# Optimization experiments

Measured on AMD Instinct MI355X. Metric: run time of the kernel, lower is better.

The kernel has to match this reference:

```python
import jax, jax.numpy as jnp
import numpy as np

NUM_EMBEDDINGS = 1024
EMBEDDING_SIZE = 256


def setup_inputs() -> dict:
    key = jax.random.key(0)
    k1, k2 = jax.random.split(key)
    z_e = jax.random.normal(k1, (32, 32, 32, EMBEDDING_SIZE), dtype=jnp.float32)
    # original init: uniform(-limit, limit), limit = sqrt(3/num_embeddings)
    limit = np.sqrt(3.0 / NUM_EMBEDDINGS)
    embeddings = jax.random.uniform(
        k2, (NUM_EMBEDDINGS, EMBEDDING_SIZE), dtype=jnp.float32,
        minval=-limit, maxval=limit)
    return {"z_e": z_e, "embeddings": embeddings}


def reference(z_e, embeddings):
    D = embeddings.shape[1]
    z_e_flat = z_e.reshape(-1, D)  # [N, D]
    distances = (
        jnp.sum(z_e_flat * z_e_flat, axis=1, keepdims=True)
        - 2.0 * (z_e_flat @ embeddings.T)
        + jnp.sum(embeddings * embeddings, axis=1)[None, :]
    )  # [N, K]
    z = jnp.argmin(distances, axis=-1).reshape(z_e.shape[:-1])  # indices
    z_q = embeddings[z]  # gather -> same shape as z_e
    return z, z_q
```

## Files before the change

kernel.cpp:

```cpp
#include <hip/hip_runtime.h>
#include <math.h>

#define N_ROWS 32768
#define DIM 256
#define K_CODES 1024
#define MARGIN 2e-3f

typedef float f32x4v __attribute__((ext_vector_type(4)));
typedef short s16x8 __attribute__((ext_vector_type(8)));

#define WS_NEEDED ((size_t)1183748)

__device__ __forceinline__ unsigned short bf16_rne(float f) {
    unsigned int u = __float_as_uint(f);
    unsigned int r = (u + 0x7FFFu + ((u >> 16) & 1u)) >> 16;
    return (unsigned short)r;
}
__device__ __forceinline__ float bf16_f32(unsigned short h) {
    return __uint_as_float(((unsigned int)h) << 16);
}

__device__ __forceinline__ float np_block128_sumsq(const float* e) {
#pragma clang fp contract(off)
    float s[16];
#pragma unroll
    for (int l = 0; l < 16; ++l) {
        float a0 = e[l]       * e[l];
        float a1 = e[16 + l]  * e[16 + l];
        float a2 = e[32 + l]  * e[32 + l];
        float a3 = e[48 + l]  * e[48 + l];
        float a4 = e[64 + l]  * e[64 + l];
        float a5 = e[80 + l]  * e[80 + l];
        float a6 = e[96 + l]  * e[96 + l];
        float a7 = e[112 + l] * e[112 + l];
        s[l] = ((a0 + a1) + (a2 + a3)) + ((a4 + a5) + (a6 + a7));
    }
    float t1[8];
#pragma unroll
    for (int i = 0; i < 8; ++i) t1[i] = s[i] + s[i + 8];
    float t2[4];
#pragma unroll
    for (int i = 0; i < 4; ++i) t2[i] = t1[i] + t1[i + 4];
    return (t2[0] + t2[2]) + (t2[1] + t2[3]);
}

__global__ __launch_bounds__(64) void npsumsq_kernel(const float* __restrict__ src,
                                                     float* __restrict__ dst) {
    __shared__ float buf[16][257];
    const int tid = threadIdx.x;
    const int r0 = blockIdx.x * 16;
#pragma unroll
    for (int it = 0; it < 16; ++it) {
        int idx = it * 64 + tid;
        int r = idx >> 6, c4 = idx & 63;
        float4 v = ((const float4*)(src + (size_t)(r0 + r) * DIM))[c4];
        buf[r][c4 * 4 + 0] = v.x;
        buf[r][c4 * 4 + 1] = v.y;
        buf[r][c4 * 4 + 2] = v.z;
        buf[r][c4 * 4 + 3] = v.w;
    }
    __syncthreads();
    if (tid < 16) {
        const float* e = buf[tid];
        dst[r0 + tid] = np_block128_sumsq(e) + np_block128_sumsq(e + 128);
    }
}

__global__ __launch_bounds__(64) void wprep_kernel(const float* __restrict__ w,
                                                   float* __restrict__ w2,
                                                   unsigned short* __restrict__ wfrag,
                                                   int* __restrict__ flagcnt) {
    __shared__ float buf[16][257];
    const int lane = threadIdx.x;
    const int t = blockIdx.x;
    const int r0 = t * 16;
    if (t == 0 && lane == 0) flagcnt[0] = 0;
#pragma unroll
    for (int it = 0; it < 16; ++it) {
        int idx = it * 64 + lane;
        int r = idx >> 6, c4 = idx & 63;
        float4 v = ((const float4*)(w + (size_t)(r0 + r) * DIM))[c4];
        buf[r][c4 * 4 + 0] = v.x;
        buf[r][c4 * 4 + 1] = v.y;
        buf[r][c4 * 4 + 2] = v.z;
        buf[r][c4 * 4 + 3] = v.w;
    }
    __syncthreads();
    if (lane < 16) {
        const float* e = buf[lane];
        w2[r0 + lane] = np_block128_sumsq(e) + np_block128_sumsq(e + 128);
    }
    const int c = lane & 15, ko = lane >> 4;
#pragma unroll
    for (int q = 0; q < 8; ++q) {
        s16x8 hh, ll;
#pragma unroll
        for (int i = 0; i < 8; ++i) {
            float f = buf[c][q * 32 + ko * 8 + i];
            unsigned short h = bf16_rne(f);
            hh[i] = (short)h;
            ll[i] = (short)bf16_rne(f - bf16_f32(h));
        }
        unsigned short* dh = wfrag + (size_t)t * 8192 + q * 512 + lane * 8;
        *(s16x8*)dh = hh;
        *(s16x8*)(dh + 4096) = ll;
    }
}

__global__ __launch_bounds__(256, 2) void vq_mfma(
    const float* __restrict__ x, const uint4* __restrict__ wfrag4,
    const float* __restrict__ w2g, const float* __restrict__ w,
    float* __restrict__ zout, float* __restrict__ zq,
    int* __restrict__ flagcnt, int* __restrict__ flaglist) {
    __shared__ uint4 tiles[2][1024];
    __shared__ float sw2[K_CODES];
    __shared__ int widx_s[64];

    const int tid = threadIdx.x;
    const int wave = tid >> 6;
    const int lane = tid & 63;
    const int rowblk = blockIdx.x * 64;
    const int rowbase = rowblk + wave * 16;

    for (int i = tid; i < K_CODES; i += 256) sw2[i] = w2g[i];

    s16x8 ahi[8], alo[8];
    {
        const float* xr = x + (size_t)(rowbase + (lane & 15)) * DIM + (lane >> 4) * 8;
#pragma unroll
        for (int q = 0; q < 8; ++q) {
            float4 a = *(const float4*)(xr + q * 32);
            float4 b = *(const float4*)(xr + q * 32 + 4);
            float e[8] = {a.x, a.y, a.z, a.w, b.x, b.y, b.z, b.w};
#pragma unroll
            for (int i = 0; i < 8; ++i) {
                unsigned short h = bf16_rne(e[i]);
                ahi[q][i] = (short)h;
                alo[q][i] = (short)bf16_rne(e[i] - bf16_f32(h));
            }
        }
    }

    tiles[0][tid] = wfrag4[tid];
    tiles[0][tid + 256] = wfrag4[tid + 256];
    tiles[0][tid + 512] = wfrag4[tid + 512];
    tiles[0][tid + 768] = wfrag4[tid + 768];

    float b1[4], b2[4];
    int i1[4];
#pragma unroll
    for (int j = 0; j < 4; ++j) { b1[j] = INFINITY; b2[j] = INFINITY; i1[j] = 0; }

    __syncthreads();

    int cur = 0;
    for (int ct = 0; ct < 64; ++ct) {
        uint4 pf0, pf1, pf2, pf3;
        if (ct < 63) {
            const uint4* g = wfrag4 + (size_t)(ct + 1) * 1024;
            pf0 = g[tid];
            pf1 = g[tid + 256];
            pf2 = g[tid + 512];
            pf3 = g[tid + 768];
        }
        const uint4* th = tiles[cur];
        f32x4v ahh = {0.f, 0.f, 0.f, 0.f};
        f32x4v ahl = {0.f, 0.f, 0.f, 0.f};
        f32x4v alh = {0.f, 0.f, 0.f, 0.f};
#pragma unroll
        for (int q = 0; q < 8; ++q) {
            s16x8 Bh = *(const s16x8*)&th[q * 64 + lane];
            s16x8 Bl = *(const s16x8*)&th[512 + q * 64 + lane];
            ahh = __builtin_amdgcn_mfma_f32_16x16x32_bf16(ahi[q], Bh, ahh, 0, 0, 0);
            ahl = __builtin_amdgcn_mfma_f32_16x16x32_bf16(ahi[q], Bl, ahl, 0, 0, 0);
            alh = __builtin_amdgcn_mfma_f32_16x16x32_bf16(alo[q], Bh, alh, 0, 0, 0);
        }
        const int code = ct * 16 + (lane & 15);
        const float w2v = sw2[code];
#pragma unroll
        for (int j = 0; j < 4; ++j) {
            float d = (ahh[j] + ahl[j]) + alh[j];
            float s = w2v - 2.0f * d;
            if (s < b2[j]) {
                if (s < b1[j]) { b2[j] = b1[j]; b1[j] = s; i1[j] = code; }
                else b2[j] = s;
            }
        }
        if (ct < 63) {
            uint4* d = tiles[cur ^ 1];
            d[tid] = pf0;
            d[tid + 256] = pf1;
            d[tid + 512] = pf2;
            d[tid + 768] = pf3;
            cur ^= 1;
        }
        __syncthreads();
    }

#pragma unroll
    for (int m = 1; m < 16; m <<= 1) {
#pragma unroll
        for (int j = 0; j < 4; ++j) {
            float ov1 = __shfl_xor(b1[j], m);
            int oi = __shfl_xor(i1[j], m);
            float ov2 = __shfl_xor(b2[j], m);
            float nb2 = fminf(fmaxf(b1[j], ov1), fminf(b2[j], ov2));
            if (ov1 < b1[j] || (ov1 == b1[j] && oi < i1[j])) { b1[j] = ov1; i1[j] = oi; }
            b2[j] = nb2;
        }
    }
    if ((lane & 15) == 0) {
#pragma unroll
        for (int j = 0; j < 4; ++j) {
            int rl = wave * 16 + (lane >> 4) * 4 + j;
            widx_s[rl] = i1[j];
            zout[rowblk + rl] = (float)i1[j];
            if (b2[j] - b1[j] < MARGIN) {
                int slot = atomicAdd(flagcnt, 1);
                flaglist[slot] = rowblk + rl;
            }
        }
    }
    __syncthreads();

    const float4* w4 = (const float4*)w;
    float4* zq4 = (float4*)zq;
#pragma unroll
    for (int p = 0; p < 16; ++p) {
        int lin = p * 256 + tid;
        int row = lin >> 6, qq = lin & 63;
        zq4[(size_t)(rowblk + row) * 64 + qq] = w4[(size_t)widx_s[row] * 64 + qq];
    }
}

__global__ __launch_bounds__(256) void rescue_kernel(
    const float* __restrict__ x, const float* __restrict__ w,
    const float* __restrict__ w2g, const int* __restrict__ flagcnt,
    const int* __restrict__ flaglist, float* __restrict__ zout,
    float* __restrict__ zq) {
    __shared__ __align__(16) float xs[DIM];
    __shared__ float dv[256];
    __shared__ int di[256];
    __shared__ int mi_s;
    __shared__ float x2_s;
    const int tid = threadIdx.x;
    const int cnt = flagcnt[0];
    for (int f = blockIdx.x; f < cnt; f += gridDim.x) {
        const int r = flaglist[f];
        __syncthreads();
        for (int i = tid; i < DIM; i += 256) xs[i] = x[(size_t)r * DIM + i];
        __syncthreads();
        if (tid == 0)
            x2_s = np_block128_sumsq(xs) + np_block128_sumsq(xs + 128);
        __syncthreads();
        const float x2vv = x2_s;
        const float4* xs4 = (const float4*)xs;
        const float4* wr0 = (const float4*)(w + (size_t)(tid + 0 * 256) * DIM);
        const float4* wr1 = (const float4*)(w + (size_t)(tid + 1 * 256) * DIM);
        const float4* wr2 = (const float4*)(w + (size_t)(tid + 2 * 256) * DIM);
        const float4* wr3 = (const float4*)(w + (size_t)(tid + 3 * 256) * DIM);
        float acc0 = 0.f, acc1 = 0.f, acc2 = 0.f, acc3 = 0.f;
#pragma unroll 4
        for (int k4 = 0; k4 < DIM / 4; ++k4) {
            float4 xv = xs4[k4];
            float4 w0 = wr0[k4], w1 = wr1[k4], w2 = wr2[k4], w3 = wr3[k4];
            acc0 = __builtin_fmaf(xv.x, w0.x, acc0);
            acc0 = __builtin_fmaf(xv.y, w0.y, acc0);
            acc0 = __builtin_fmaf(xv.z, w0.z, acc0);
            acc0 = __builtin_fmaf(xv.w, w0.w, acc0);
            acc1 = __builtin_fmaf(xv.x, w1.x, acc1);
            acc1 = __builtin_fmaf(xv.y, w1.y, acc1);
            acc1 = __builtin_fmaf(xv.z, w1.z, acc1);
            acc1 = __builtin_fmaf(xv.w, w1.w, acc1);
            acc2 = __builtin_fmaf(xv.x, w2.x, acc2);
            acc2 = __builtin_fmaf(xv.y, w2.y, acc2);
            acc2 = __builtin_fmaf(xv.z, w2.z, acc2);
            acc2 = __builtin_fmaf(xv.w, w2.w, acc2);
            acc3 = __builtin_fmaf(xv.x, w3.x, acc3);
            acc3 = __builtin_fmaf(xv.y, w3.y, acc3);
            acc3 = __builtin_fmaf(xv.z, w3.z, acc3);
            acc3 = __builtin_fmaf(xv.w, w3.w, acc3);
        }
        float bv = INFINITY;
        int bi = 0;
        float accs[4] = {acc0, acc1, acc2, acc3};
#pragma unroll
        for (int cc = 0; cc < 4; ++cc) {
            int c = tid + cc * 256;
            float s = (x2vv - 2.0f * accs[cc]) + w2g[c];
            if (s < bv) { bv = s; bi = c; }
        }
        dv[tid] = bv;
        di[tid] = bi;
        __syncthreads();
        if (tid == 0) {
            float mv = dv[0];
            int mi = di[0];
            for (int t = 1; t < 256; ++t)
                if (dv[t] < mv || (dv[t] == mv && di[t] < mi)) { mv = dv[t]; mi = di[t]; }
            zout[r] = (float)mi;
            mi_s = mi;
        }
        __syncthreads();
        zq[(size_t)r * DIM + tid] = w[(size_t)mi_s * DIM + tid];
    }
}

#define BM 64
#define BN 128
#define BK 64
#define LDX 68

__global__ __launch_bounds__(256) void vq_kernel_lds(
    const float* __restrict__ x, const float* __restrict__ w,
    const float* __restrict__ x2g, const float* __restrict__ w2g,
    float* __restrict__ zout, float* __restrict__ zq) {
    __shared__ float xs[BM * LDX];
    __shared__ float ws_[BN * LDX];
    __shared__ float sw2[K_CODES];
    __shared__ float sx2[BM];
    __shared__ int widx[BM];

    const int tid = threadIdx.x;
    const int bm0 = blockIdx.x * BM;
    const int rg = tid & 15;
    const int cg = tid >> 4;

    for (int i = tid; i < K_CODES; i += 256) sw2[i] = w2g[i];
    if (tid < BM) sx2[tid] = x2g[bm0 + tid];

    float best[4];
    int bidx[4];
#pragma unroll
    for (int i = 0; i < 4; ++i) { best[i] = INFINITY; bidx[i] = 0; }

    const float4* x4 = (const float4*)x;
    const float4* w4 = (const float4*)w;

    for (int cn = 0; cn < K_CODES / BN; ++cn) {
        float acc[4][8];
#pragma unroll
        for (int i = 0; i < 4; ++i)
#pragma unroll
            for (int j = 0; j < 8; ++j) acc[i][j] = 0.f;

        for (int dk = 0; dk < DIM / BK; ++dk) {
            __syncthreads();
#pragma unroll
            for (int p = 0; p < 4; ++p) {
                int l = p * 256 + tid;
                int row = l >> 4, c4 = l & 15;
                float4 v = x4[(size_t)(bm0 + row) * (DIM / 4) + dk * (BK / 4) + c4];
                *(float4*)&xs[row * LDX + c4 * 4] = v;
            }
#pragma unroll
            for (int p = 0; p < 8; ++p) {
                int l = p * 256 + tid;
                int row = l >> 4, c4 = l & 15;
                float4 v = w4[(size_t)(cn * BN + row) * (DIM / 4) + dk * (BK / 4) + c4];
                *(float4*)&ws_[row * LDX + c4 * 4] = v;
            }
            __syncthreads();
#pragma unroll
            for (int d = 0; d < BK; d += 4) {
                float4 xv[4], wv[8];
#pragma unroll
                for (int i = 0; i < 4; ++i)
                    xv[i] = *(const float4*)&xs[(rg + 16 * i) * LDX + d];
#pragma unroll
                for (int j = 0; j < 8; ++j)
                    wv[j] = *(const float4*)&ws_[(cg + 16 * j) * LDX + d];
#pragma unroll
                for (int i = 0; i < 4; ++i)
#pragma unroll
                    for (int j = 0; j < 8; ++j) {
                        acc[i][j] = __builtin_fmaf(xv[i].x, wv[j].x, acc[i][j]);
                        acc[i][j] = __builtin_fmaf(xv[i].y, wv[j].y, acc[i][j]);
                        acc[i][j] = __builtin_fmaf(xv[i].z, wv[j].z, acc[i][j]);
                        acc[i][j] = __builtin_fmaf(xv[i].w, wv[j].w, acc[i][j]);
                    }
            }
        }
#pragma unroll
        for (int j = 0; j < 8; ++j) {
            int c = cn * BN + cg + 16 * j;
            float w2v = sw2[c];
#pragma unroll
            for (int i = 0; i < 4; ++i) {
                float t = sx2[rg + 16 * i] - 2.0f * acc[i][j];
                float s = t + w2v;
                if (s < best[i]) { best[i] = s; bidx[i] = c; }
            }
        }
    }

    __syncthreads();
    float* sval = xs;
    int* sidx = (int*)(xs + 64 * 17);
#pragma unroll
    for (int i = 0; i < 4; ++i) {
        sval[(rg + 16 * i) * 17 + cg] = best[i];
        sidx[(rg + 16 * i) * 17 + cg] = bidx[i];
    }
    __syncthreads();
    if (tid < BM) {
        float bv = INFINITY;
        int bi = 0;
        for (int c = 0; c < 16; ++c) {
            float v = sval[tid * 17 + c];
            int id = sidx[tid * 17 + c];
            if (v < bv || (v == bv && id < bi)) { bv = v; bi = id; }
        }
        widx[tid] = bi;
        zout[bm0 + tid] = (float)bi;
    }
    __syncthreads();
    float4* zq4 = (float4*)zq;
#pragma unroll
    for (int p = 0; p < 16; ++p) {
        int lin = p * 256 + tid;
        int row = lin >> 6, q = lin & 63;
        zq4[(size_t)(bm0 + row) * 64 + q] = w4[(size_t)widx[row] * 64 + q];
    }
}

extern "C" void kernel_launch(void* const* d_in, const int* in_sizes, int n_in,
                              void* d_out, int out_size, void* d_ws, size_t ws_size,
                              hipStream_t stream) {
    const float* z_e = (const float*)d_in[0];
    const float* emb = (const float*)d_in[1];
    float* x2g = (float*)d_ws;
    int* flaglist = (int*)d_ws;
    float* w2g = x2g + N_ROWS;
    unsigned short* wfrag = (unsigned short*)(w2g + K_CODES);
    int* flagcnt = (int*)(wfrag + (size_t)2 * K_CODES * DIM);
    float* zout = (float*)d_out;
    float* zq = (float*)d_out + N_ROWS;

    if (ws_size >= WS_NEEDED) {
        wprep_kernel<<<K_CODES / 16, 64, 0, stream>>>(emb, w2g, wfrag, flagcnt);
        vq_mfma<<<N_ROWS / 64, 256, 0, stream>>>(z_e, (const uint4*)wfrag, w2g,
                                                 emb, zout, zq, flagcnt, flaglist);
        rescue_kernel<<<256, 256, 0, stream>>>(z_e, emb, w2g, flagcnt,
                                               flaglist, zout, zq);
    } else {
        npsumsq_kernel<<<N_ROWS / 16, 64, 0, stream>>>(z_e, x2g);
        npsumsq_kernel<<<K_CODES / 16, 64, 0, stream>>>(emb, w2g);
        vq_kernel_lds<<<N_ROWS / BM, 256, 0, stream>>>(z_e, emb, x2g, w2g, zout, zq);
    }
}
```

Baseline: 132.2 us.

## Read codebook fragments directly from global memory, drop LDS tiles and block barriers

Removes the double-buffered LDS staging of codebook fragments and the shared w2 table. Each wave now reads B fragments and w2 values straight from global memory, relying on L1/L2 caching. All block-level barriers go away and the gather epilogue becomes per-wave. This cuts LDS traffic, synchronisation stalls and LDS footprint, which may raise occupancy. In exchange, every wave issues redundant global loads and MFMAs may stall on global latency with no explicit prefetch.

Result: slower. 208.3 us (+57.6%).

```diff
diff --git a/kernel.cpp b/kernel.cpp
--- a/kernel.cpp
+++ b/kernel.cpp
@@ -112,17 +112,12 @@
     const float* __restrict__ w2g, const float* __restrict__ w,
     float* __restrict__ zout, float* __restrict__ zq,
     int* __restrict__ flagcnt, int* __restrict__ flaglist) {
-    __shared__ uint4 tiles[2][1024];
-    __shared__ float sw2[K_CODES];
-    __shared__ int widx_s[64];
+    __shared__ int widx_s[4][16];
 
     const int tid = threadIdx.x;
     const int wave = tid >> 6;
     const int lane = tid & 63;
-    const int rowblk = blockIdx.x * 64;
-    const int rowbase = rowblk + wave * 16;
-
-    for (int i = tid; i < K_CODES; i += 256) sw2[i] = w2g[i];
+    const int rowbase = blockIdx.x * 64 + wave * 16;
 
     s16x8 ahi[8], alo[8];
     {
@@ -141,29 +136,13 @@
         }
     }
 
-    tiles[0][tid] = wfrag4[tid];
-    tiles[0][tid + 256] = wfrag4[tid + 256];
-    tiles[0][tid + 512] = wfrag4[tid + 512];
-    tiles[0][tid + 768] = wfrag4[tid + 768];
-
     float b1[4], b2[4];
     int i1[4];
 #pragma unroll
     for (int j = 0; j < 4; ++j) { b1[j] = INFINITY; b2[j] = INFINITY; i1[j] = 0; }
 
-    __syncthreads();
-
-    int cur = 0;
     for (int ct = 0; ct < 64; ++ct) {
-        uint4 pf0, pf1, pf2, pf3;
-        if (ct < 63) {
-            const uint4* g = wfrag4 + (size_t)(ct + 1) * 1024;
-            pf0 = g[tid];
-            pf1 = g[tid + 256];
-            pf2 = g[tid + 512];
-            pf3 = g[tid + 768];
-        }
-        const uint4* th = tiles[cur];
+        const uint4* th = wfrag4 + (size_t)ct * 1024;
         f32x4v ahh = {0.f, 0.f, 0.f, 0.f};
         f32x4v ahl = {0.f, 0.f, 0.f, 0.f};
         f32x4v alh = {0.f, 0.f, 0.f, 0.f};
@@ -176,7 +155,7 @@
             alh = __builtin_amdgcn_mfma_f32_16x16x32_bf16(alo[q], Bh, alh, 0, 0, 0);
         }
         const int code = ct * 16 + (lane & 15);
-        const float w2v = sw2[code];
+        const float w2v = w2g[code];
 #pragma unroll
         for (int j = 0; j < 4; ++j) {
             float d = (ahh[j] + ahl[j]) + alh[j];
@@ -186,15 +165,6 @@
                 else b2[j] = s;
             }
         }
-        if (ct < 63) {
-            uint4* d = tiles[cur ^ 1];
-            d[tid] = pf0;
-            d[tid + 256] = pf1;
-            d[tid + 512] = pf2;
-            d[tid + 768] = pf3;
-            cur ^= 1;
-        }
-        __syncthreads();
     }
 
 #pragma unroll
@@ -212,24 +182,24 @@
     if ((lane & 15) == 0) {
 #pragma unroll
         for (int j = 0; j < 4; ++j) {
-            int rl = wave * 16 + (lane >> 4) * 4 + j;
-            widx_s[rl] = i1[j];
-            zout[rowblk + rl] = (float)i1[j];
+            int rl = (lane >> 4) * 4 + j;
+            widx_s[wave][rl] = i1[j];
+            zout[rowbase + rl] = (float)i1[j];
             if (b2[j] - b1[j] < MARGIN) {
                 int slot = atomicAdd(flagcnt, 1);
-                flaglist[slot] = rowblk + rl;
-            }
-        }
-    }
-    __syncthreads();
+                flaglist[slot] = rowbase + rl;
+            }
+        }
+    }
+    __builtin_amdgcn_wave_barrier();
 
     const float4* w4 = (const float4*)w;
     float4* zq4 = (float4*)zq;
 #pragma unroll
     for (int p = 0; p < 16; ++p) {
-        int lin = p * 256 + tid;
+        int lin = p * 64 + lane;
         int row = lin >> 6, qq = lin & 63;
-        zq4[(size_t)(rowblk + row) * 64 + qq] = w4[(size_t)widx_s[row] * 64 + qq];
+        zq4[(size_t)(rowbase + row) * 64 + qq] = w4[(size_t)widx_s[wave][row] * 64 + qq];
     }
 }
 
```

## Fuse near-tie rescue pass into the MFMA kernel and widen weight prep blocks

Applied to the files above, without the earlier changes.

Removes the separate rescue kernel and its global flag counter and list. Each MFMA block now recomputes its own ambiguous rows in exact fp32 before writing indices and the gathered codebook rows, which saves one kernel launch, the global atomics, and rewriting zout/zq for rescued rows. The weight prep kernel moves from 64 to 256 threads per block, spreading the fragment packing across four waves. The cost is extra LDS in the main kernel, which may reduce occupancy, and the rescue work now runs serially inside blocks that happen to have flagged rows.

New measurement: 239.5 us. 81.2% more time.

```diff
diff --git a/kernel.cpp b/kernel.cpp
--- a/kernel.cpp
+++ b/kernel.cpp
@@ -9,7 +9,7 @@
 typedef float f32x4v __attribute__((ext_vector_type(4)));
 typedef short s16x8 __attribute__((ext_vector_type(8)));
 
-#define WS_NEEDED ((size_t)1183748)
+#define WS_NEEDED ((size_t)1183744)
 
 __device__ __forceinline__ unsigned short bf16_rne(float f) {
     unsigned int u = __float_as_uint(f);
@@ -66,18 +66,18 @@
     }
 }
 
-__global__ __launch_bounds__(64) void wprep_kernel(const float* __restrict__ w,
-                                                   float* __restrict__ w2,
-                                                   unsigned short* __restrict__ wfrag,
-                                                   int* __restrict__ flagcnt) {
+__global__ __launch_bounds__(256) void wprep_kernel(const float* __restrict__ w,
+                                                    float* __restrict__ w2,
+                                                    unsigned short* __restrict__ wfrag) {
     __shared__ float buf[16][257];
-    const int lane = threadIdx.x;
+    const int tid = threadIdx.x;
+    const int lane = tid & 63;
+    const int sw = tid >> 6;
     const int t = blockIdx.x;
     const int r0 = t * 16;
-    if (t == 0 && lane == 0) flagcnt[0] = 0;
-#pragma unroll
-    for (int it = 0; it < 16; ++it) {
-        int idx = it * 64 + lane;
+#pragma unroll
+    for (int it = 0; it < 4; ++it) {
+        int idx = it * 256 + tid;
         int r = idx >> 6, c4 = idx & 63;
         float4 v = ((const float4*)(w + (size_t)(r0 + r) * DIM))[c4];
         buf[r][c4 * 4 + 0] = v.x;
@@ -86,13 +86,14 @@
         buf[r][c4 * 4 + 3] = v.w;
     }
     __syncthreads();
-    if (lane < 16) {
-        const float* e = buf[lane];
-        w2[r0 + lane] = np_block128_sumsq(e) + np_block128_sumsq(e + 128);
+    if (tid < 16) {
+        const float* e = buf[tid];
+        w2[r0 + tid] = np_block128_sumsq(e) + np_block128_sumsq(e + 128);
     }
     const int c = lane & 15, ko = lane >> 4;
 #pragma unroll
-    for (int q = 0; q < 8; ++q) {
+    for (int qq = 0; qq < 2; ++qq) {
+        const int q = sw * 2 + qq;
         s16x8 hh, ll;
 #pragma unroll
         for (int i = 0; i < 8; ++i) {
@@ -110,11 +111,16 @@
 __global__ __launch_bounds__(256, 2) void vq_mfma(
     const float* __restrict__ x, const uint4* __restrict__ wfrag4,
     const float* __restrict__ w2g, const float* __restrict__ w,
-    float* __restrict__ zout, float* __restrict__ zq,
-    int* __restrict__ flagcnt, int* __restrict__ flaglist) {
+    float* __restrict__ zout, float* __restrict__ zq) {
     __shared__ uint4 tiles[2][1024];
     __shared__ float sw2[K_CODES];
     __shared__ int widx_s[64];
+    __shared__ int flagrows[64];
+    __shared__ int nflag;
+    __shared__ __align__(16) float xs[DIM];
+    __shared__ float dv[256];
+    __shared__ int di[256];
+    __shared__ float x2_s;
 
     const int tid = threadIdx.x;
     const int wave = tid >> 6;
@@ -122,6 +128,7 @@
     const int rowblk = blockIdx.x * 64;
     const int rowbase = rowblk + wave * 16;
 
+    if (tid == 0) nflag = 0;
     for (int i = tid; i < K_CODES; i += 256) sw2[i] = w2g[i];
 
     s16x8 ahi[8], alo[8];
@@ -214,41 +221,18 @@
         for (int j = 0; j < 4; ++j) {
             int rl = wave * 16 + (lane >> 4) * 4 + j;
             widx_s[rl] = i1[j];
-            zout[rowblk + rl] = (float)i1[j];
             if (b2[j] - b1[j] < MARGIN) {
-                int slot = atomicAdd(flagcnt, 1);
-                flaglist[slot] = rowblk + rl;
-            }
-        }
-    }
-    __syncthreads();
-
-    const float4* w4 = (const float4*)w;
-    float4* zq4 = (float4*)zq;
-#pragma unroll
-    for (int p = 0; p < 16; ++p) {
-        int lin = p * 256 + tid;
-        int row = lin >> 6, qq = lin & 63;
-        zq4[(size_t)(rowblk + row) * 64 + qq] = w4[(size_t)widx_s[row] * 64 + qq];
-    }
-}
-
-__global__ __launch_bounds__(256) void rescue_kernel(
-    const float* __restrict__ x, const float* __restrict__ w,
-    const float* __restrict__ w2g, const int* __restrict__ flagcnt,
-    const int* __restrict__ flaglist, float* __restrict__ zout,
-    float* __restrict__ zq) {
-    __shared__ __align__(16) float xs[DIM];
-    __shared__ float dv[256];
-    __shared__ int di[256];
-    __shared__ int mi_s;
-    __shared__ float x2_s;
-    const int tid = threadIdx.x;
-    const int cnt = flagcnt[0];
-    for (int f = blockIdx.x; f < cnt; f += gridDim.x) {
-        const int r = flaglist[f];
-        __syncthreads();
-        for (int i = tid; i < DIM; i += 256) xs[i] = x[(size_t)r * DIM + i];
+                int slot = atomicAdd(&nflag, 1);
+                flagrows[slot] = rl;
+            }
+        }
+    }
+    __syncthreads();
+
+    for (int f = 0; f < nflag; ++f) {
+        const int rl = flagrows[f];
+        const int r = rowblk + rl;
+        xs[tid] = x[(size_t)r * DIM + tid];
         __syncthreads();
         if (tid == 0)
             x2_s = np_block128_sumsq(xs) + np_block128_sumsq(xs + 128);
@@ -298,11 +282,20 @@
             int mi = di[0];
             for (int t = 1; t < 256; ++t)
                 if (dv[t] < mv || (dv[t] == mv && di[t] < mi)) { mv = dv[t]; mi = di[t]; }
-            zout[r] = (float)mi;
-            mi_s = mi;
+            widx_s[rl] = mi;
         }
         __syncthreads();
-        zq[(size_t)r * DIM + tid] = w[(size_t)mi_s * DIM + tid];
+    }
+
+    if (tid < 64) zout[rowblk + tid] = (float)widx_s[tid];
+
+    const float4* w4 = (const float4*)w;
+    float4* zq4 = (float4*)zq;
+#pragma unroll
+    for (int p = 0; p < 16; ++p) {
+        int lin = p * 256 + tid;
+        int row = lin >> 6, qq = lin & 63;
+        zq4[(size_t)(rowblk + row) * 64 + qq] = w4[(size_t)widx_s[row] * 64 + qq];
     }
 }
 
@@ -430,19 +423,15 @@
     const float* z_e = (const float*)d_in[0];
     const float* emb = (const float*)d_in[1];
     float* x2g = (float*)d_ws;
-    int* flaglist = (int*)d_ws;
     float* w2g = x2g + N_ROWS;
     unsigned short* wfrag = (unsigned short*)(w2g + K_CODES);
-    int* flagcnt = (int*)(wfrag + (size_t)2 * K_CODES * DIM);
     float* zout = (float*)d_out;
     float* zq = (float*)d_out + N_ROWS;
 
     if (ws_size >= WS_NEEDED) {
-        wprep_kernel<<<K_CODES / 16, 64, 0, stream>>>(emb, w2g, wfrag, flagcnt);
+        wprep_kernel<<<K_CODES / 16, 256, 0, stream>>>(emb, w2g, wfrag);
         vq_mfma<<<N_ROWS / 64, 256, 0, stream>>>(z_e, (const uint4*)wfrag, w2g,
-                                                 emb, zout, zq, flagcnt, flaglist);
-        rescue_kernel<<<256, 256, 0, stream>>>(z_e, emb, w2g, flagcnt,
-                                               flaglist, zout, zq);
+                                                 emb, zout, zq);
     } else {
         npsumsq_kernel<<<N_ROWS / 16, 64, 0, stream>>>(z_e, x2g);
         npsumsq_kernel<<<K_CODES / 16, 64, 0, stream>>>(emb, w2g);
```
